# Optimization experiments

Measured on AMD Instinct MI355X. Metric: run time of the kernel, lower is better.

Reference implementation:

```python
import jax, jax.numpy as jnp
import numpy as np

B, Q, K, DQ, DK, H, DV = 4, 1024, 1024, 256, 256, 64, 256

def setup_inputs() -> dict:
    key = jax.random.key(0)
    k1, k2, k3, k4, k5, k6 = jax.random.split(key, 6)
    queries = jax.random.normal(k1, (B, Q, DQ), dtype=jnp.float32)
    keys = jax.random.normal(k2, (B, K, DK), dtype=jnp.float32)
    values = jax.random.normal(k3, (B, K, DV), dtype=jnp.float32)
    # learned params (stored as (in, out) so x @ W matches nn.Linear)
    W_q = jax.random.normal(k4, (DQ, H), dtype=jnp.float32) / np.sqrt(DQ)
    W_k = jax.random.normal(k5, (DK, H), dtype=jnp.float32) / np.sqrt(DK)
    w_v = jax.random.normal(k6, (H,), dtype=jnp.float32) / np.sqrt(H)
    return {"queries": queries, "keys": keys, "values": values,
            "W_q": W_q, "W_k": W_k, "w_v": w_v}

def reference(queries, keys, values, W_q, W_k, w_v):
    # projections: [B,Q,H], [B,K,H]
    q = jnp.einsum('bqd,dh->bqh', queries, W_q)
    k = jnp.einsum('bkd,dh->bkh', keys, W_k)
    # broadcast add -> tanh -> reduce with w_v: scores [B,Q,K]
    features = jnp.tanh(q[:, :, None, :] + k[:, None, :, :])  # [B,Q,K,H]
    scores = jnp.einsum('bqkh,h->bqk', features, w_v)
    attn = jax.nn.softmax(scores, axis=-1)  # dropout is identity in eval
    return jnp.einsum('bqk,bkv->bqv', attn, values)
```

## Files before the change

kernel.cpp:

```cpp
#include <hip/hip_runtime.h>

#define Bn 4
#define Qn 1024
#define Kn 1024
#define Dd 256
#define Hh 64
#define Dv 256
#define TQ 16

typedef __attribute__((ext_vector_type(8))) short short8;
typedef __attribute__((ext_vector_type(4))) float floatx4;
typedef __attribute__((ext_vector_type(2))) float floatx2;

__device__ __forceinline__ floatx2 fma2(floatx2 a, floatx2 b, floatx2 c) {
    return __builtin_elementwise_fma(a, b, c);
}
__device__ __forceinline__ floatx2 mk2(float x, float y) {
    floatx2 r; r.x = x; r.y = y; return r;
}

__device__ __forceinline__ short f32_to_bf16(float x) {
    unsigned u = __float_as_uint(x);
    unsigned r = u + 0x7fffu + ((u >> 16) & 1u);
    return (short)(r >> 16);
}
__device__ __forceinline__ float bf16_to_f32(short h) {
    return __uint_as_float(((unsigned)(unsigned short)h) << 16);
}

__global__ __launch_bounds__(256) void prep_kernel(const float* __restrict__ Xq,
                                                   const float* __restrict__ Wq,
                                                   const float* __restrict__ Xk,
                                                   const float* __restrict__ Wk,
                                                   const float* __restrict__ V,
                                                   float* __restrict__ Eq,
                                                   float* __restrict__ Ekt,
                                                   short* __restrict__ Vhi,
                                                   short* __restrict__ Vlo) {
    __shared__ __align__(16) char smem[65536];
    int t = threadIdx.x;
    if (blockIdx.x < 128) {
        short* wh_lds = (short*)smem;
        short* wl_lds = (short*)(smem + 32768);
        int side = blockIdx.x >> 6;
        const float* X = side ? Xk : Xq;
        const float* W = side ? Wk : Wq;
        #pragma unroll
        for (int si = 0; si < 8; ++si) {
            int s = t * 8 + si;
            int l = s & 63, ct = (s >> 6) & 3, kt = s >> 8;
            int col = ct * 16 + (l & 15);
            int kb = kt * 32 + (l >> 4) * 8;
            short8 hi, lo;
            #pragma unroll
            for (int j = 0; j < 8; ++j) {
                float x = W[(kb + j) * Hh + col];
                short hs = f32_to_bf16(x);
                hi[j] = hs;
                lo[j] = f32_to_bf16(x - bf16_to_f32(hs));
            }
            *(short8*)(wh_lds + s * 8) = hi;
            *(short8*)(wl_lds + s * 8) = lo;
        }
        __syncthreads();
        int wave = t >> 6, l = t & 63;
        int r0 = ((blockIdx.x & 63) * 4 + wave) * 16;
        const float* xrow = X + (size_t)(r0 + (l & 15)) * Dd + (l >> 4) * 8;
        short8 ah[8], al[8];
        #pragma unroll
        for (int kt = 0; kt < 8; ++kt) {
            floatx4 a = *(const floatx4*)(xrow + kt * 32);
            floatx4 b = *(const floatx4*)(xrow + kt * 32 + 4);
            #pragma unroll
            for (int j = 0; j < 4; ++j) {
                short hs = f32_to_bf16(a[j]);
                ah[kt][j] = hs;
                al[kt][j] = f32_to_bf16(a[j] - bf16_to_f32(hs));
                short hs2 = f32_to_bf16(b[j]);
                ah[kt][j + 4] = hs2;
                al[kt][j + 4] = f32_to_bf16(b[j] - bf16_to_f32(hs2));
            }
        }
        floatx4 acc[4];
        #pragma unroll
        for (int ct = 0; ct < 4; ++ct) acc[ct] = (floatx4){0.f, 0.f, 0.f, 0.f};
        #pragma unroll
        for (int kt = 0; kt < 8; ++kt) {
            #pragma unroll
            for (int ct = 0; ct < 4; ++ct) {
                short8 wh = *(const short8*)(wh_lds + ((kt * 4 + ct) * 64 + l) * 8);
                short8 wl = *(const short8*)(wl_lds + ((kt * 4 + ct) * 64 + l) * 8);
                acc[ct] = __builtin_amdgcn_mfma_f32_16x16x32_bf16(ah[kt], wh, acc[ct], 0, 0, 0);
                acc[ct] = __builtin_amdgcn_mfma_f32_16x16x32_bf16(al[kt], wh, acc[ct], 0, 0, 0);
                acc[ct] = __builtin_amdgcn_mfma_f32_16x16x32_bf16(ah[kt], wl, acc[ct], 0, 0, 0);
            }
        }
        #pragma unroll
        for (int ct = 0; ct < 4; ++ct) {
            #pragma unroll
            for (int i = 0; i < 4; ++i) {
                float e = __expf(2.f * acc[ct][i]);
                int row = r0 + (l >> 4) * 4 + i;
                int h = ct * 16 + (l & 15);
                if (!side) {
                    Eq[(size_t)row * Hh + h] = e;
                } else {
                    int b = row >> 10, k = row & 1023;
                    Ekt[((size_t)b * Hh + h) * Kn + k] = e;
                }
            }
        }
    } else {
        float* tile = (float*)smem;
        int blk = blockIdx.x - 128;
        int b = blk >> 5;
        int kt = blk & 31;
        const float* Vg = V + (b * Kn + kt * 32) * Dv;
        for (int i = 0; i < 8; ++i) {
            int k = i * 4 + (t >> 6);
            int n4 = (t & 63) * 4;
            float4 v = *(const float4*)(Vg + k * Dv + n4);
            tile[k * 261 + n4 + 0] = v.x;
            tile[k * 261 + n4 + 1] = v.y;
            tile[k * 261 + n4 + 2] = v.z;
            tile[k * 261 + n4 + 3] = v.w;
        }
        __syncthreads();
        int wave = t >> 6, l = t & 63;
        int n_in = l & 15, kc = l >> 4;
        for (int p = 0; p < 4; ++p) {
            int nt = wave * 4 + p;
            int n = nt * 16 + n_in;
            short8 hi, lo;
            #pragma unroll
            for (int j = 0; j < 8; ++j) {
                float x = tile[(kc * 8 + j) * 261 + n];
                short hs = f32_to_bf16(x);
                hi[j] = hs;
                lo[j] = f32_to_bf16(x - bf16_to_f32(hs));
            }
            size_t base = (((size_t)(b * 32 + kt) * 16 + nt) * 512) + (size_t)l * 8;
            *(short8*)(Vhi + base) = hi;
            *(short8*)(Vlo + base) = lo;
        }
    }
}

__global__ __launch_bounds__(1024, 4) void attn_kernel(const float* __restrict__ Eq,
                                                       const float* __restrict__ Ekt,
                                                       const short* __restrict__ Vhi,
                                                       const short* __restrict__ Vlo,
                                                       const float* __restrict__ wv,
                                                       float* __restrict__ out) {
    __shared__ __align__(16) unsigned sc[TQ * 1028];
    __shared__ float wsum[16 * TQ];
    __shared__ float rinv_s[TQ];

    int tid = threadIdx.x;
    int blk = blockIdx.x;
    int b = (blk & 7) >> 1;
    int tile = (blk >> 3) * 2 + (blk & 1);
    int qbase = tile * TQ;

    const float* kb = Ekt + (size_t)b * Hh * Kn;
    const float* qp = Eq + (size_t)(b * Qn + qbase) * Hh;
    const float4* wv4 = (const float4*)wv;
    floatx2 s2[TQ / 2];
    #pragma unroll
    for (int i = 0; i < TQ / 2; ++i) { s2[i].x = 0.f; s2[i].y = 0.f; }

    float e0 = kb[0 * Kn + tid];
    float e1 = kb[1 * Kn + tid];
    float e2 = kb[2 * Kn + tid];
    float e3 = kb[3 * Kn + tid];
    floatx2 one2 = mk2(1.f, 1.f);
    for (int h4 = 0; h4 < Hh / 4; ++h4) {
        float n0, n1, n2, n3;
        if (h4 < Hh / 4 - 1) {
            const float* kn = kb + (h4 + 1) * 4 * Kn;
            n0 = kn[0 * Kn + tid];
            n1 = kn[1 * Kn + tid];
            n2 = kn[2 * Kn + tid];
            n3 = kn[3 * Kn + tid];
        }
        float4 w4 = wv4[h4];
        floatx2 e0s = mk2(e0, e0), e1s = mk2(e1, e1);
        floatx2 e2s = mk2(e2, e2), e3s = mk2(e3, e3);
        floatx2 wx = mk2(w4.x, w4.x), wy = mk2(w4.y, w4.y);
        floatx2 wz = mk2(w4.z, w4.z), ww = mk2(w4.w, w4.w);
        #pragma unroll
        for (int qq = 0; qq < TQ; qq += 2) {
            float4 qva = *(const float4*)(qp + qq * Hh + h4 * 4);
            float4 qvb = *(const float4*)(qp + (qq + 1) * Hh + h4 * 4);
            floatx2 A = fma2(mk2(qva.x, qvb.x), e0s, one2);
            floatx2 B = fma2(mk2(qva.y, qvb.y), e1s, one2);
            floatx2 C = fma2(mk2(qva.z, qvb.z), e2s, one2);
            floatx2 D = fma2(mk2(qva.w, qvb.w), e3s, one2);
            floatx2 AB = A * B;
            floatx2 CD = C * D;
            floatx2 ABCD = AB * CD;
            floatx2 NAB = fma2(wx, B, wy * A);
            floatx2 NCD = fma2(wz, D, ww * C);
            floatx2 NUM = fma2(NCD, AB, NAB * CD);
            floatx2 R = mk2(__builtin_amdgcn_rcpf(ABCD.x),
                            __builtin_amdgcn_rcpf(ABCD.y));
            s2[qq >> 1] = fma2(NUM, R, s2[qq >> 1]);
        }
        e0 = n0; e1 = n1; e2 = n2; e3 = n3;
    }

    unsigned short* sp = (unsigned short*)sc;
    float part[TQ];
    #pragma unroll
    for (int q = 0; q < TQ; ++q) {
        float sq = (q & 1) ? s2[q >> 1].y : s2[q >> 1].x;
        float p = __expf(-2.f * sq);
        part[q] = p;
        short hs = f32_to_bf16(p);
        sp[q * 2056 + tid] = (unsigned short)hs;
        sp[q * 2056 + 1024 + tid] = (unsigned short)f32_to_bf16(p - bf16_to_f32(hs));
    }

    int wave = tid >> 6, lane = tid & 63;
    #pragma unroll
    for (int q = 0; q < TQ; ++q) {
        #pragma unroll
        for (int off = 32; off >= 1; off >>= 1)
            part[q] += __shfl_xor(part[q], off, 64);
    }
    if (lane == 0) {
        #pragma unroll
        for (int q = 0; q < TQ; ++q) wsum[wave * TQ + q] = part[q];
    }
    __syncthreads();

    {
        float v = (lane < 16) ? wsum[lane * TQ + wave] : 0.f;
        v += __shfl_xor(v, 8, 64);
        v += __shfl_xor(v, 4, 64);
        v += __shfl_xor(v, 2, 64);
        v += __shfl_xor(v, 1, 64);
        if (lane == 0) rinv_s[wave] = 1.f / v;
    }
    __syncthreads();

    int qf = lane & 15, kc = lane >> 4;
    floatx4 acc = {0.f, 0.f, 0.f, 0.f};
    const char* scb = (const char*)sc;
    for (int kt = 0; kt < 32; ++kt) {
        short8 bhi = *(const short8*)(scb + qf * 4112 + kt * 64 + kc * 16);
        short8 blo = *(const short8*)(scb + qf * 4112 + 2048 + kt * 64 + kc * 16);
        size_t base = (((size_t)(b * 32 + kt) * 16 + wave) * 512) + (size_t)lane * 8;
        short8 ah = *(const short8*)(Vhi + base);
        short8 al = *(const short8*)(Vlo + base);
        acc = __builtin_amdgcn_mfma_f32_16x16x32_bf16(ah, bhi, acc, 0, 0, 0);
        acc = __builtin_amdgcn_mfma_f32_16x16x32_bf16(al, bhi, acc, 0, 0, 0);
        acc = __builtin_amdgcn_mfma_f32_16x16x32_bf16(ah, blo, acc, 0, 0, 0);
    }
    {
        float r = rinv_s[qf];
        float* ob = out + ((size_t)(b * Qn + qbase + qf)) * Dv + wave * 16 + kc * 4;
        float4 o = { acc[0] * r, acc[1] * r, acc[2] * r, acc[3] * r };
        *(float4*)ob = o;
    }
}

extern "C" void kernel_launch(void* const* d_in, const int* in_sizes, int n_in,
                              void* d_out, int out_size, void* d_ws, size_t ws_size,
                              hipStream_t stream) {
    const float* queries = (const float*)d_in[0];
    const float* keys    = (const float*)d_in[1];
    const float* values  = (const float*)d_in[2];
    const float* W_q     = (const float*)d_in[3];
    const float* W_k     = (const float*)d_in[4];
    const float* w_v     = (const float*)d_in[5];
    float* out = (float*)d_out;

    float* Eq  = (float*)d_ws;
    float* Ekt = Eq + Bn * Qn * Hh;
    short* Vhi = (short*)(Ekt + Bn * Kn * Hh);
    short* Vlo = Vhi + (size_t)Bn * Kn * Dv;

    prep_kernel<<<256, 256, 0, stream>>>(queries, W_q, keys, W_k, values,
                                         Eq, Ekt, Vhi, Vlo);
    attn_kernel<<<Bn * (Qn / TQ), 1024, 0, stream>>>(Eq, Ekt, Vhi, Vlo, w_v, out);
}
```

Measured before the change: 115.3 us.

## Halve query tile to 8 for more attention blocks and vectorize Ekt stores

Reduces the query tile per attention block from 16 to 8, doubling the block count and raising the occupancy hint to 8 blocks per CU, so more work runs in parallel and each block needs less LDS. The 16-wide MFMA now duplicates query rows, so half of its output is wasted and only lanes with qf<8 write. The prep kernel also remaps the weight-conversion loop so global reads of W are coalesced, and writes Ekt as float4 instead of scalar stores. The main risk is the wasted MFMA work and having to re-read V tiles twice as often in total.

```diff
diff --git a/kernel.cpp b/kernel.cpp
--- a/kernel.cpp
+++ b/kernel.cpp
@@ -6,7 +6,7 @@
 #define Dd 256
 #define Hh 64
 #define Dv 256
-#define TQ 16
+#define TQ 8
 
 typedef __attribute__((ext_vector_type(8))) short short8;
 typedef __attribute__((ext_vector_type(4))) float floatx4;
@@ -45,12 +45,12 @@
         int side = blockIdx.x >> 6;
         const float* X = side ? Xk : Xq;
         const float* W = side ? Wk : Wq;
+        int wave = t >> 6, l = t & 63;
         #pragma unroll
         for (int si = 0; si < 8; ++si) {
-            int s = t * 8 + si;
-            int l = s & 63, ct = (s >> 6) & 3, kt = s >> 8;
-            int col = ct * 16 + (l & 15);
-            int kb = kt * 32 + (l >> 4) * 8;
+            int s = si * 256 + t;
+            int col = wave * 16 + (l & 15);
+            int kb = si * 32 + (l >> 4) * 8;
             short8 hi, lo;
             #pragma unroll
             for (int j = 0; j < 8; ++j) {
@@ -63,7 +63,6 @@
             *(short8*)(wl_lds + s * 8) = lo;
         }
         __syncthreads();
-        int wave = t >> 6, l = t & 63;
         int r0 = ((blockIdx.x & 63) * 4 + wave) * 16;
         const float* xrow = X + (size_t)(r0 + (l & 15)) * Dd + (l >> 4) * 8;
         short8 ah[8], al[8];
@@ -97,17 +96,21 @@
         }
         #pragma unroll
         for (int ct = 0; ct < 4; ++ct) {
-            #pragma unroll
-            for (int i = 0; i < 4; ++i) {
-                float e = __expf(2.f * acc[ct][i]);
-                int row = r0 + (l >> 4) * 4 + i;
-                int h = ct * 16 + (l & 15);
-                if (!side) {
-                    Eq[(size_t)row * Hh + h] = e;
-                } else {
-                    int b = row >> 10, k = row & 1023;
-                    Ekt[((size_t)b * Hh + h) * Kn + k] = e;
-                }
+            int h = ct * 16 + (l & 15);
+            float e0 = __expf(2.f * acc[ct][0]);
+            float e1 = __expf(2.f * acc[ct][1]);
+            float e2 = __expf(2.f * acc[ct][2]);
+            float e3 = __expf(2.f * acc[ct][3]);
+            int row0g = r0 + (l >> 4) * 4;
+            if (!side) {
+                Eq[(size_t)(row0g + 0) * Hh + h] = e0;
+                Eq[(size_t)(row0g + 1) * Hh + h] = e1;
+                Eq[(size_t)(row0g + 2) * Hh + h] = e2;
+                Eq[(size_t)(row0g + 3) * Hh + h] = e3;
+            } else {
+                int b = row0g >> 10, k0 = row0g & 1023;
+                float4 o = { e0, e1, e2, e3 };
+                *(float4*)(Ekt + ((size_t)(b * Hh + h)) * Kn + k0) = o;
             }
         }
     } else {
@@ -146,7 +149,7 @@
     }
 }
 
-__global__ __launch_bounds__(1024, 4) void attn_kernel(const float* __restrict__ Eq,
+__global__ __launch_bounds__(1024, 8) void attn_kernel(const float* __restrict__ Eq,
                                                        const float* __restrict__ Ekt,
                                                        const short* __restrict__ Vhi,
                                                        const short* __restrict__ Vlo,
@@ -234,7 +237,7 @@
     }
     __syncthreads();
 
-    {
+    if (wave < TQ) {
         float v = (lane < 16) ? wsum[lane * TQ + wave] : 0.f;
         v += __shfl_xor(v, 8, 64);
         v += __shfl_xor(v, 4, 64);
@@ -245,11 +248,12 @@
     __syncthreads();
 
     int qf = lane & 15, kc = lane >> 4;
+    int qd = qf & (TQ - 1);
     floatx4 acc = {0.f, 0.f, 0.f, 0.f};
     const char* scb = (const char*)sc;
     for (int kt = 0; kt < 32; ++kt) {
-        short8 bhi = *(const short8*)(scb + qf * 4112 + kt * 64 + kc * 16);
-        short8 blo = *(const short8*)(scb + qf * 4112 + 2048 + kt * 64 + kc * 16);
+        short8 bhi = *(const short8*)(scb + qd * 4112 + kt * 64 + kc * 16);
+        short8 blo = *(const short8*)(scb + qd * 4112 + 2048 + kt * 64 + kc * 16);
         size_t base = (((size_t)(b * 32 + kt) * 16 + wave) * 512) + (size_t)lane * 8;
         short8 ah = *(const short8*)(Vhi + base);
         short8 al = *(const short8*)(Vlo + base);
@@ -257,8 +261,8 @@
         acc = __builtin_amdgcn_mfma_f32_16x16x32_bf16(al, bhi, acc, 0, 0, 0);
         acc = __builtin_amdgcn_mfma_f32_16x16x32_bf16(ah, blo, acc, 0, 0, 0);
     }
-    {
-        float r = rinv_s[qf];
+    if (qf < TQ) {
+        float r = rinv_s[qd];
         float* ob = out + ((size_t)(b * Qn + qbase + qf)) * Dv + wave * 16 + kc * 4;
         float4 o = { acc[0] * r, acc[1] * r, acc[2] * r, acc[3] * r };
         *(float4*)ob = o;
```

New measurement: 114.5 us. No clear change (-0.7%).
